# Kernel tuning notes

Measured on AMD Instinct MI355X. Metric: run time of the kernel, lower is better.

Reference implementation:

```python
import jax, jax.numpy as jnp
import numpy as np

WINDOW = 2


def _fo_pool(h, f):
    """c_t = f_t * c_{t-1} + (1 - f_t) * h_t with c_{-1} = 0, scanned over axis 1 (time).
    Implemented as an associative scan on affine maps (a, b): c -> a*c + b."""
    def combine(left, right):
        a1, b1 = left
        a2, b2 = right
        return a2 * a1, a2 * b1 + b2
    a = f
    b = (1.0 - f) * h
    _, c = jax.lax.associative_scan(combine, (a, b), axis=1)
    return c


def setup_inputs() -> dict:
    key = jax.random.key(0)
    k1, k2 = jax.random.split(key)
    B, T, C, U = 8, 2048, 1024, 1024
    x = jax.random.normal(k1, (B, T, C), dtype=jnp.float32)
    # Keras Conv1D kernel layout: [window, in_channels, out_channels]; glorot-ish scale
    scale = (2.0 / (C + 3 * U)) ** 0.5
    kernel = jax.random.normal(k2, (WINDOW, C, 3 * U), dtype=jnp.float32) * scale
    bias = jnp.zeros((3 * U,), dtype=jnp.float32)
    return {"x": x, "kernel": kernel, "bias": bias}


def reference(x, kernel, bias):
    # causal conv1d: pad (window-1) on the left of time axis
    gv = jax.lax.conv_general_dilated(
        x, kernel,
        window_strides=(1,),
        padding=[(WINDOW - 1, 0)],
        dimension_numbers=("NWC", "WIO", "NWC"),
    ) + bias  # [B, T, 3U]
    hidden, forget, output = jnp.split(gv, 3, axis=-1)
    hidden = jnp.tanh(hidden)
    forget = jax.nn.sigmoid(forget)
    c = _fo_pool(hidden, forget)           # [B, T, U]
    h = jax.nn.sigmoid(output) * c          # output gate
    return h
```

## Files before the change

### kernel.cpp

```cpp
#include <hip/hip_runtime.h>


typedef _Float16 f16;
typedef _Float16 f16x8 __attribute__((ext_vector_type(8)));
typedef float    f32x4 __attribute__((ext_vector_type(4)));

#define Bq 8
#define Tq 2048
#define Cq 1024
#define Uq 1024
#define Mq (Bq*Tq)
#define Kq (2*Cq)
#define Nq (3*Uq)
#define NCH 32
#define CHL (Tq/NCH)

#define AS1 __attribute__((address_space(1)))
#define AS3 __attribute__((address_space(3)))

__global__ void prep_xs(const float* __restrict__ x, f16* __restrict__ Xs) {
    long long idx = ((long long)blockIdx.x * blockDim.x + threadIdx.x) * 8;
    int c = (int)(idx & (Cq - 1));
    long long row = idx >> 10;
    int tp = (int)(row % (Tq + 1));
    int b  = (int)(row / (Tq + 1));
    f16x8 o;
    if (tp == 0) {
#pragma unroll
        for (int j = 0; j < 8; j++) o[j] = (f16)0.0f;
    } else {
        const float* src = x + (((size_t)b * Tq + (tp - 1)) << 10) + c;
        float4 v0 = *(const float4*)(src);
        float4 v1 = *(const float4*)(src + 4);
        o[0]=(f16)v0.x; o[1]=(f16)v0.y; o[2]=(f16)v0.z; o[3]=(f16)v0.w;
        o[4]=(f16)v1.x; o[5]=(f16)v1.y; o[6]=(f16)v1.z; o[7]=(f16)v1.w;
    }
    *(f16x8*)(Xs + idx) = o;
}

__global__ void prep_wt(const float* __restrict__ w, f16* __restrict__ WT) {
    __shared__ float t[32][33];
    int kb = blockIdx.x * 32, nb = blockIdx.y * 32;
    int tx = threadIdx.x & 31, ty = threadIdx.x >> 5;
#pragma unroll
    for (int j = 0; j < 32; j += 8)
        t[ty + j][tx] = w[(size_t)(kb + ty + j) * Nq + nb + tx];
    __syncthreads();
#pragma unroll
    for (int j = 0; j < 32; j += 8)
        WT[(size_t)(nb + ty + j) * Kq + kb + tx] = (f16)t[tx][ty + j];
}

__global__ __launch_bounds__(512, 2) void gemm_gates8(
    const f16* __restrict__ Xs, const f16* __restrict__ WT,
    const float* __restrict__ bias,
    f16* __restrict__ H, f16* __restrict__ F, f16* __restrict__ O)
{
    __shared__ __align__(16) f16 smem[65536];
    const int tid  = threadIdx.x;
    const int lane = tid & 63;
    const int wave = tid >> 6;
    const int wm = wave >> 2;
    const int wn = wave & 3;

    const int wg  = blockIdx.x;
    const int swz = (wg & 7) * 96 + (wg >> 3);
    const int mT  = swz / 12, nT = swz - mT * 12;
    const int rM  = mT * 256;
    const int nB  = nT * 256;
    const int b   = rM >> 11;
    const int t0  = rM & (Tq - 1);
    const size_t xsRow0 = (size_t)b * (Tq + 1) + t0;

    const int srow = tid >> 3;
    const int scol = (((tid & 7) ^ (srow & 7))) * 8;
    const f16* Abase = Xs + (xsRow0 + srow) * (size_t)Cq + scol;
    const f16* Bbase = WT + (size_t)(nB + srow) * Kq + scol;
    const int dstT = tid * 16;

#define STAGE_A(c, h, kt) do { \
    const f16* _s = Abase + (size_t)((h) * 128) * Cq + (kt) * 64; \
    int _d = (c) * 65536 + (h) * 16384 + dstT; \
    __builtin_amdgcn_global_load_lds((const AS1 void*)_s, \
        (AS3 void*)((char*)smem + _d), 16, 0, 0); \
    __builtin_amdgcn_global_load_lds((const AS1 void*)(_s + (size_t)64 * Cq), \
        (AS3 void*)((char*)smem + _d + 8192), 16, 0, 0); \
} while (0)

#define STAGE_B(c, h, kt) do { \
    const f16* _s = Bbase + (size_t)((h) * 128) * Kq + (kt) * 64; \
    int _d = 32768 + (c) * 65536 + (h) * 16384 + dstT; \
    __builtin_amdgcn_global_load_lds((const AS1 void*)_s, \
        (AS3 void*)((char*)smem + _d), 16, 0, 0); \
    __builtin_amdgcn_global_load_lds((const AS1 void*)(_s + (size_t)64 * Kq), \
        (AS3 void*)((char*)smem + _d + 8192), 16, 0, 0); \
} while (0)

    const int rAoff = (wm * 64 + (lane & 15)) * 128;
    const int rBoff = (wn * 32 + (lane & 15)) * 128;
    const int ksw0 = (((lane >> 4) * 16)) ^ ((lane & 7) << 4);
    const int ksw1 = (64 + ((lane >> 4) * 16)) ^ ((lane & 7) << 4);

    f32x4 acc[2][2][4][2] = {};
    f16x8 afA[4][2], afB[4][2], bg0[2][2], bg1[2][2];

#define LOADA_TO(c, h, dst) do { \
    const char* _a = (const char*)smem + (c) * 65536 + (h) * 16384 + rAoff; \
    _Pragma("unroll") \
    for (int mi = 0; mi < 4; mi++) { \
        dst[mi][0] = *(const f16x8*)(_a + mi * 2048 + ksw0); \
        dst[mi][1] = *(const f16x8*)(_a + mi * 2048 + ksw1); \
    } \
} while (0)

#define LOADB_TO(c, g, breg) do { \
    const char* _b = (const char*)smem + 32768 + (c) * 65536 + (g) * 16384 + rBoff; \
    _Pragma("unroll") \
    for (int ni = 0; ni < 2; ni++) { \
        breg[ni][0] = *(const f16x8*)(_b + ni * 2048 + ksw0); \
        breg[ni][1] = *(const f16x8*)(_b + ni * 2048 + ksw1); \
    } \
} while (0)

#define MM(h, g, afr, breg) do { \
    _Pragma("unroll") \
    for (int ks = 0; ks < 2; ks++) \
    _Pragma("unroll") \
    for (int mi = 0; mi < 4; mi++) \
    _Pragma("unroll") \
    for (int ni = 0; ni < 2; ni++) \
        acc[h][g][mi][ni] = __builtin_amdgcn_mfma_f32_16x16x32_f16(afr[mi][ks], breg[ni][ks], acc[h][g][mi][ni], 0, 0, 0); \
} while (0)

#define BAR()  __builtin_amdgcn_s_barrier()
#define SB0()  __builtin_amdgcn_sched_barrier(0)
#define PRIO1  __builtin_amdgcn_s_setprio(1)
#define PRIO0  __builtin_amdgcn_s_setprio(0)
#define LGKMC(n) asm volatile("s_waitcnt lgkmcnt(" #n ")" ::: "memory")
#define VMC(n)   asm volatile("s_waitcnt vmcnt(" #n ")" ::: "memory")

#define KTILE(c, ktn) do { \
     LOADB_TO(c, 1, bg1); STAGE_A(1 - (c), 0, ktn); STAGE_B(1 - (c), 0, ktn); \
           SB0(); LGKMC(4); SB0(); \
           PRIO1; MM(0, 0, afA, bg0); PRIO0; \
           VMC(4); BAR(); \
     LOADA_TO(c, 1, afB); STAGE_B(1 - (c), 1, ktn); STAGE_A(1 - (c), 1, ktn); \
           SB0(); LGKMC(8); SB0(); \
           PRIO1; MM(0, 1, afA, bg1); PRIO0; \
     SB0(); LGKMC(0); SB0(); \
           PRIO1; MM(1, 0, afB, bg0); PRIO0; \
           VMC(4); BAR(); \
     LOADA_TO(1 - (c), 0, afA); LOADB_TO(1 - (c), 0, bg0); \
           SB0(); LGKMC(12); SB0(); \
           PRIO1; MM(1, 1, afB, bg1); PRIO0; \
           VMC(2); BAR(); \
} while (0)

    STAGE_A(0, 0, 0); STAGE_B(0, 0, 0); STAGE_B(0, 1, 0); STAGE_A(0, 1, 0);
    VMC(0);
    BAR();
    LOADA_TO(0, 0, afA); LOADB_TO(0, 0, bg0);

    for (int t = 0; t < 32; t += 2) {
        KTILE(0, t + 1);
        KTILE(1, t + 2);
    }

    const int gate = nB >> 10;
    f16* G = (gate == 0) ? H : ((gate == 1) ? F : O);
#pragma unroll
    for (int h = 0; h < 2; h++)
#pragma unroll
    for (int g = 0; g < 2; g++)
#pragma unroll
    for (int ni = 0; ni < 2; ni++) {
        const int col = nB + g * 128 + wn * 32 + ni * 16 + (lane & 15);
        const int u = col & (Uq - 1);
        const float bv = bias[col];
#pragma unroll
        for (int mi = 0; mi < 4; mi++)
#pragma unroll
        for (int j = 0; j < 4; j++) {
            const int row = rM + h * 128 + wm * 64 + mi * 16 + ((lane >> 4) << 2) + j;
            float v = acc[h][g][mi][ni][j] + bv;
            float r;
            if (gate == 0) r = 1.0f - 2.0f / (__expf(2.0f * v) + 1.0f);
            else           r = 1.0f / (1.0f + __expf(-v));
            G[(size_t)row * Uq + u] = (f16)r;
        }
    }
}

__global__ void scan_pass1(const f16* __restrict__ F, const f16* __restrict__ H,
                           float* __restrict__ Ach, float* __restrict__ Bch) {
    int idx = blockIdx.x * blockDim.x + threadIdx.x;
    int u  = idx & (Uq - 1);
    int ch = (idx >> 10) & (NCH - 1);
    int b  = idx >> 15;
    size_t base = ((size_t)b * Tq + ch * CHL) * Uq + u;
    float a = 1.0f, c = 0.0f;
    for (int i = 0; i < CHL; i++) {
        float f = (float)F[base + (size_t)i * Uq];
        float h = (float)H[base + (size_t)i * Uq];
        c = f * c + (1.0f - f) * h;
        a *= f;
    }
    Ach[idx] = a;
    Bch[idx] = c;
}

__global__ void scan_pass2(const float* __restrict__ Ach, const float* __restrict__ Bch,
                           float* __restrict__ Cin) {
    int idx = blockIdx.x * blockDim.x + threadIdx.x;
    int u = idx & (Uq - 1);
    int b = idx >> 10;
    float c = 0.0f;
    for (int ch = 0; ch < NCH; ch++) {
        int o = ((b * NCH) + ch) * Uq + u;
        Cin[o] = c;
        c = Ach[o] * c + Bch[o];
    }
}

__global__ void scan_pass3(const f16* __restrict__ F, const f16* __restrict__ H,
                           const f16* __restrict__ O, const float* __restrict__ Cin,
                           float* __restrict__ out) {
    int idx = blockIdx.x * blockDim.x + threadIdx.x;
    int u  = idx & (Uq - 1);
    int ch = (idx >> 10) & (NCH - 1);
    int b  = idx >> 15;
    size_t base = ((size_t)b * Tq + ch * CHL) * Uq + u;
    float c = Cin[idx];
    for (int i = 0; i < CHL; i++) {
        float f = (float)F[base + (size_t)i * Uq];
        float h = (float)H[base + (size_t)i * Uq];
        c = f * c + (1.0f - f) * h;
        out[base + (size_t)i * Uq] = (float)O[base + (size_t)i * Uq] * c;
    }
}

extern "C" void kernel_launch(void* const* d_in, const int* in_sizes, int n_in,
                              void* d_out, int out_size, void* d_ws, size_t ws_size,
                              hipStream_t stream) {
    const float* x    = (const float*)d_in[0];
    const float* w    = (const float*)d_in[1];
    const float* bias = (const float*)d_in[2];
    float* out = (float*)d_out;
    char* ws = (char*)d_ws;

    f16* Xs   = (f16*)(ws);
    f16* WT   = (f16*)(ws + 33570816);
    f16* Hh   = (f16*)(ws + 46153728);
    f16* Fh   = (f16*)(ws + 79708160);
    f16* Oh   = (f16*)(ws + 113262592);
    float* Ach = (float*)(ws + 146817024);
    float* Bch = (float*)(ws + 147865600);
    float* Cin = (float*)(ws + 148914176);

    prep_xs<<<(Bq * (Tq + 1) * Cq) / (8 * 256), 256, 0, stream>>>(x, Xs);
    prep_wt<<<dim3(Kq / 32, Nq / 32), 256, 0, stream>>>(w, WT);
    gemm_gates8<<<(Mq / 256) * (Nq / 256), 512, 0, stream>>>(Xs, WT, bias, Hh, Fh, Oh);
    scan_pass1<<<(Bq * NCH * Uq) / 256, 256, 0, stream>>>(Fh, Hh, Ach, Bch);
    scan_pass2<<<(Bq * Uq) / 256, 256, 0, stream>>>(Ach, Bch, Cin);
    scan_pass3<<<(Bq * NCH * Uq) / 256, 256, 0, stream>>>(Fh, Hh, Oh, Cin, out);
}
```

Before: 258.6 us.

## Reschedule GEMM LDS fragment loads and fold scan pass2 into pass3

The GEMM inner K-tile schedule is reordered so the A-fragment LDS reads are split into partial chunks and interleaved with the MFMA groups. Barrier and vmcnt placement moves accordingly, with tighter lgkmcnt waits, to hide LDS latency behind matrix math. Separately, the small scan_pass2 kernel is removed. Each pass3 thread now recomputes its chunk carry-in by serially combining the preceding chunk summaries, which saves a launch and the Cin round trip at the cost of redundant reads of Ach/Bch.

```diff
diff --git a/kernel.cpp b/kernel.cpp
--- a/kernel.cpp
+++ b/kernel.cpp
@@ -104,10 +104,10 @@
     f32x4 acc[2][2][4][2] = {};
     f16x8 afA[4][2], afB[4][2], bg0[2][2], bg1[2][2];
 
-#define LOADA_TO(c, h, dst) do { \
+#define LOADA_PART(c, h, dst, mlo, mhi) do { \
     const char* _a = (const char*)smem + (c) * 65536 + (h) * 16384 + rAoff; \
     _Pragma("unroll") \
-    for (int mi = 0; mi < 4; mi++) { \
+    for (int mi = (mlo); mi < (mhi); mi++) { \
         dst[mi][0] = *(const f16x8*)(_a + mi * 2048 + ksw0); \
         dst[mi][1] = *(const f16x8*)(_a + mi * 2048 + ksw1); \
     } \
@@ -140,26 +140,28 @@
 #define VMC(n)   asm volatile("s_waitcnt vmcnt(" #n ")" ::: "memory")
 
 #define KTILE(c, ktn) do { \
-     LOADB_TO(c, 1, bg1); STAGE_A(1 - (c), 0, ktn); STAGE_B(1 - (c), 0, ktn); \
-           SB0(); LGKMC(4); SB0(); \
+     LOADB_TO(c, 1, bg1); LOADA_PART(c, 1, afB, 0, 1); \
+           STAGE_A(1 - (c), 0, ktn); STAGE_B(1 - (c), 0, ktn); \
+           SB0(); LGKMC(6); SB0(); \
            PRIO1; MM(0, 0, afA, bg0); PRIO0; \
-           VMC(4); BAR(); \
-     LOADA_TO(c, 1, afB); STAGE_B(1 - (c), 1, ktn); STAGE_A(1 - (c), 1, ktn); \
+     LOADA_PART(c, 1, afB, 1, 4); \
+           STAGE_B(1 - (c), 1, ktn); STAGE_A(1 - (c), 1, ktn); \
            SB0(); LGKMC(8); SB0(); \
            PRIO1; MM(0, 1, afA, bg1); PRIO0; \
-     SB0(); LGKMC(0); SB0(); \
+           VMC(4); BAR(); \
+     LOADA_PART(1 - (c), 0, afA, 0, 3); \
+           SB0(); LGKMC(6); SB0(); \
            PRIO1; MM(1, 0, afB, bg0); PRIO0; \
-           VMC(4); BAR(); \
-     LOADA_TO(1 - (c), 0, afA); LOADB_TO(1 - (c), 0, bg0); \
-           SB0(); LGKMC(12); SB0(); \
+     LOADA_PART(1 - (c), 0, afA, 3, 4); LOADB_TO(1 - (c), 0, bg0); \
+           SB0(); \
            PRIO1; MM(1, 1, afB, bg1); PRIO0; \
-           VMC(2); BAR(); \
+           VMC(0); BAR(); \
 } while (0)
 
     STAGE_A(0, 0, 0); STAGE_B(0, 0, 0); STAGE_B(0, 1, 0); STAGE_A(0, 1, 0);
     VMC(0);
     BAR();
-    LOADA_TO(0, 0, afA); LOADB_TO(0, 0, bg0);
+    LOADA_PART(0, 0, afA, 0, 4); LOADB_TO(0, 0, bg0);
 
     for (int t = 0; t < 32; t += 2) {
         KTILE(0, t + 1);
@@ -209,28 +211,21 @@
     Bch[idx] = c;
 }
 
-__global__ void scan_pass2(const float* __restrict__ Ach, const float* __restrict__ Bch,
-                           float* __restrict__ Cin) {
-    int idx = blockIdx.x * blockDim.x + threadIdx.x;
-    int u = idx & (Uq - 1);
-    int b = idx >> 10;
-    float c = 0.0f;
-    for (int ch = 0; ch < NCH; ch++) {
-        int o = ((b * NCH) + ch) * Uq + u;
-        Cin[o] = c;
-        c = Ach[o] * c + Bch[o];
-    }
-}
-
 __global__ void scan_pass3(const f16* __restrict__ F, const f16* __restrict__ H,
-                           const f16* __restrict__ O, const float* __restrict__ Cin,
+                           const f16* __restrict__ O,
+                           const float* __restrict__ Ach, const float* __restrict__ Bch,
                            float* __restrict__ out) {
     int idx = blockIdx.x * blockDim.x + threadIdx.x;
     int u  = idx & (Uq - 1);
     int ch = (idx >> 10) & (NCH - 1);
     int b  = idx >> 15;
+    int cbase = (b * NCH) * Uq + u;
+    float c = 0.0f;
+    for (int ch2 = 0; ch2 < ch; ch2++) {
+        int o = cbase + ch2 * Uq;
+        c = Ach[o] * c + Bch[o];
+    }
     size_t base = ((size_t)b * Tq + ch * CHL) * Uq + u;
-    float c = Cin[idx];
     for (int i = 0; i < CHL; i++) {
         float f = (float)F[base + (size_t)i * Uq];
         float h = (float)H[base + (size_t)i * Uq];
@@ -255,12 +250,10 @@
     f16* Oh   = (f16*)(ws + 113262592);
     float* Ach = (float*)(ws + 146817024);
     float* Bch = (float*)(ws + 147865600);
-    float* Cin = (float*)(ws + 148914176);
 
     prep_xs<<<(Bq * (Tq + 1) * Cq) / (8 * 256), 256, 0, stream>>>(x, Xs);
     prep_wt<<<dim3(Kq / 32, Nq / 32), 256, 0, stream>>>(w, WT);
     gemm_gates8<<<(Mq / 256) * (Nq / 256), 512, 0, stream>>>(Xs, WT, bias, Hh, Fh, Oh);
     scan_pass1<<<(Bq * NCH * Uq) / 256, 256, 0, stream>>>(Fh, Hh, Ach, Bch);
-    scan_pass2<<<(Bq * Uq) / 256, 256, 0, stream>>>(Ach, Bch, Cin);
-    scan_pass3<<<(Bq * NCH * Uq) / 256, 256, 0, stream>>>(Fh, Hh, Oh, Cin, out);
-}
+    scan_pass3<<<(Bq * NCH * Uq) / 256, 256, 0, stream>>>(Fh, Hh, Oh, Ach, Bch, out);
+}
```

Result: no change. 254.9 us (-1.4%).
